# Optimization experiments

Measured on AMD Instinct MI355X. Metric: run time of the kernel, lower is better.

Reference implementation:

```python
import jax, jax.numpy as jnp
import numpy as np

B, H, W, C = 32, 32, 32, 768
E = 4          # num_experts
TOPK = 2
HD = int(C * 0.25)  # 192, expert hidden dim


def setup_inputs() -> dict:
    key = jax.random.key(0)
    ks = jax.random.split(key, 7)
    x = jax.random.normal(ks[0], (B, H, W, C), dtype=jnp.float32)
    # router: nn.Linear(C, E), weight [E, C] init N(0, 0.02), bias zeros
    router_w = jax.random.normal(ks[1], (E, C), dtype=jnp.float32) * 0.02
    router_b = jnp.zeros((E,), dtype=jnp.float32)
    # per-expert MLP: fc1 [E, HD, C], fc2 [E, C, HD] (torch Linear weight layout)
    fc1_w = jax.random.normal(ks[2], (E, HD, C), dtype=jnp.float32) * (1.0 / np.sqrt(C))
    fc1_b = jax.random.normal(ks[3], (E, HD), dtype=jnp.float32) * 0.01
    fc2_w = jax.random.normal(ks[4], (E, C, HD), dtype=jnp.float32) * (1.0 / np.sqrt(HD))
    fc2_b = jax.random.normal(ks[5], (E, C), dtype=jnp.float32) * 0.01
    return {"x": x, "router_w": router_w, "router_b": router_b,
            "fc1_w": fc1_w, "fc1_b": fc1_b, "fc2_w": fc2_w, "fc2_b": fc2_b}


def reference(x, router_w, router_b, fc1_w, fc1_b, fc2_w, fc2_b):
    b, h, w, c = x.shape
    xt = x.reshape(b, h * w, c)                              # [B, S, C]
    # --- router: softmax + top-k + renormalize ---
    logits = jnp.einsum('bsc,ec->bse', xt, router_w) + router_b
    probs = jax.nn.softmax(logits, axis=-1)                  # [B, S, E]
    topk_w, topk_idx = jax.lax.top_k(probs, TOPK)            # [B, S, K]
    topk_w = topk_w / (jnp.sum(topk_w, axis=-1, keepdims=True) + 1e-8)
    # per-expert combine weight: sum over k of weight where idx==e -> [B, S, E]
    combine = jnp.sum(jax.nn.one_hot(topk_idx, E, dtype=xt.dtype)
                      * topk_w[..., None], axis=-2)          # [B, S, E]
    # --- all experts densely (same math as masked gather/scatter) ---
    # fc1 + exact GELU: [B, S, E, HD]
    hmid = jax.nn.gelu(jnp.einsum('bsc,ehc->bseh', xt, fc1_w) + fc1_b,
                       approximate=False)
    # weight tokens before fc2 to avoid [B,S,E,C] intermediate
    hw = hmid * combine[..., None]                           # [B, S, E, HD]
    out = jnp.einsum('bseh,ech->bsc', hw, fc2_w)
    out = out + jnp.einsum('bse,ec->bsc', combine, fc2_b)    # weighted fc2 bias
    return out.reshape(b, h, w, c)
```

## Files before the change

kernel.cpp:

```cpp
#include <hip/hip_runtime.h>
#include <hip/hip_bf16.h>
#include <math.h>

typedef __attribute__((ext_vector_type(8))) __bf16 bf16x8;
typedef __attribute__((ext_vector_type(4))) float f32x4;
typedef __attribute__((ext_vector_type(4))) unsigned short u16x4;

#define TOKENS 32768
#define CDIM   768
#define NKDIM  768

__device__ __forceinline__ void async_copy16(const void* g, void* l) {
    __builtin_amdgcn_global_load_lds(
        (const __attribute__((address_space(1))) void*)g,
        (__attribute__((address_space(3))) void*)l, 16, 0, 0);
}

__device__ __forceinline__ float fast_gelu(float v) {
    float x  = v * 0.70710678118654752f;
    float ax = fabsf(x);
    float t  = __builtin_amdgcn_rcpf(1.0f + 0.3275911f * ax);
    float poly = t * (0.254829592f +
                 t * (-0.284496736f +
                 t * (1.421413741f +
                 t * (-1.453152027f +
                 t * 1.061405429f))));
    float erfv = 1.0f - poly * __expf(-x * x);
    erfv = copysignf(erfv, x);
    return 0.5f * v * (1.0f + erfv);
}

__global__ __launch_bounds__(256) void prep_weights(
    const float* __restrict__ fc1w, const float* __restrict__ fc2w,
    __hip_bfloat16* __restrict__ b1, __hip_bfloat16* __restrict__ b2t)
{
    int idx = blockIdx.x * 256 + threadIdx.x;
    if (idx >= 768 * 768) return;
    b1[idx] = __float2bfloat16(fc1w[idx]);
    int c = idx / 768;
    int r = idx - c * 768;
    int e = r / 192;
    int h = r - e * 192;
    b2t[idx] = __float2bfloat16(fc2w[((size_t)e * 768 + c) * 192 + h]);
}

__global__ __launch_bounds__(256) void router_convert(
    const float* __restrict__ x, const float* __restrict__ rw,
    const float* __restrict__ rb,
    __hip_bfloat16* __restrict__ xb, float* __restrict__ comb)
{
    int wave = threadIdx.x >> 6;
    int lane = threadIdx.x & 63;
    int token = blockIdx.x * 4 + wave;

    const float* xr = x + (size_t)token * CDIM + lane * 12;
    float4 v0 = *(const float4*)(xr);
    float4 v1 = *(const float4*)(xr + 4);
    float4 v2 = *(const float4*)(xr + 8);

    float vals[12];
    *(float4*)(vals) = v0; *(float4*)(vals + 4) = v1; *(float4*)(vals + 8) = v2;
    alignas(16) __hip_bfloat16 hb[12];
#pragma unroll
    for (int j = 0; j < 12; ++j) hb[j] = __float2bfloat16(vals[j]);
    u16x4* dst = (u16x4*)((unsigned short*)xb + (size_t)token * CDIM + lane * 12);
    dst[0] = ((u16x4*)hb)[0];
    dst[1] = ((u16x4*)hb)[1];
    dst[2] = ((u16x4*)hb)[2];

    float s[4];
#pragma unroll
    for (int e = 0; e < 4; ++e) {
        const float* w = rw + e * CDIM + lane * 12;
        float4 w0 = *(const float4*)(w);
        float4 w1 = *(const float4*)(w + 4);
        float4 w2 = *(const float4*)(w + 8);
        s[e] = v0.x * w0.x + v0.y * w0.y + v0.z * w0.z + v0.w * w0.w
             + v1.x * w1.x + v1.y * w1.y + v1.z * w1.z + v1.w * w1.w
             + v2.x * w2.x + v2.y * w2.y + v2.z * w2.z + v2.w * w2.w;
    }
#pragma unroll
    for (int e = 0; e < 4; ++e) {
        float v = s[e];
        v += __shfl_xor(v, 32); v += __shfl_xor(v, 16); v += __shfl_xor(v, 8);
        v += __shfl_xor(v, 4);  v += __shfl_xor(v, 2);  v += __shfl_xor(v, 1);
        s[e] = v;
    }
    float lg[4], p[4];
#pragma unroll
    for (int e = 0; e < 4; ++e) lg[e] = s[e] + rb[e];
    float mx = fmaxf(fmaxf(lg[0], lg[1]), fmaxf(lg[2], lg[3]));
    float ps = 0.f;
#pragma unroll
    for (int e = 0; e < 4; ++e) { p[e] = __expf(lg[e] - mx); ps += p[e]; }
#pragma unroll
    for (int e = 0; e < 4; ++e) p[e] /= ps;
    int a = 0;
#pragma unroll
    for (int e = 1; e < 4; ++e) if (p[e] > p[a]) a = e;
    int b = (a == 0) ? 1 : 0;
#pragma unroll
    for (int e = 0; e < 4; ++e) if (e != a && p[e] > p[b]) b = e;
    float wsum = p[a] + p[b] + 1e-8f;
    float cb[4] = {0.f, 0.f, 0.f, 0.f};
    cb[a] = p[a] / wsum;
    cb[b] = p[b] / wsum;
    if (lane == 0) {
        float4 o; o.x = cb[0]; o.y = cb[1]; o.z = cb[2]; o.w = cb[3];
        *(float4*)(comb + (size_t)token * 4) = o;
    }
}

#define BM 128
#define BN 128
#define BK 64

template <int MODE, int K>
__global__ __launch_bounds__(256) void gemm_bt(
    const __hip_bfloat16* __restrict__ A, const __hip_bfloat16* __restrict__ Bt,
    const float* __restrict__ comb,
    const float* __restrict__ bias1,
    const float* __restrict__ bias2,
    __hip_bfloat16* __restrict__ HW,
    float* __restrict__ OUT)
{
    __shared__ __hip_bfloat16 smem[BM * BK * 4];

    const int tid = threadIdx.x;
    const int wave = tid >> 6, lane = tid & 63;
    const int wm = (wave >> 1) * 64, wn = (wave & 1) * 64;
    const int lrow = lane & 15, quad = lane >> 4;

    const int g = blockIdx.x;
    const int xcd = g & 7;
    const int slot = g >> 3;
    const int byg = slot / 6;
    const int bx = slot - byg * 6;
    const int by = (xcd << 5) + byg;
    const int rowB0 = bx * BN;
    const int rowA0 = by * BM;

    const int srow = lane >> 3;
    const int scol = ((lane & 7) ^ srow) * 8;

    size_t aoff[4];
    __hip_bfloat16* ldsA[4];
#pragma unroll
    for (int p = 0; p < 4; ++p) {
        int c = wave * 4 + p;
        aoff[p] = (size_t)(c * 8 + srow) * K + scol;
        ldsA[p] = smem + c * 8 * BK;
    }
    const __hip_bfloat16* Abase = A + (size_t)rowA0 * K;
    const __hip_bfloat16* Bbase = Bt + (size_t)rowB0 * K;

    auto stage = [&](int buf, int k0) {
        int boff = buf * (2 * BM * BK);
#pragma unroll
        for (int p = 0; p < 4; ++p) {
            async_copy16(Abase + aoff[p] + k0, ldsA[p] + boff);
            async_copy16(Bbase + aoff[p] + k0, ldsA[p] + boff + BM * BK);
        }
    };

    f32x4 acc[4][4] = {};
    constexpr int NIT = K / BK;

    stage(0, 0);
    __syncthreads();
#pragma unroll
    for (int it = 0; it < NIT; ++it) {
        if (it + 1 < NIT) stage((it + 1) & 1, (it + 1) * BK);
        const __hip_bfloat16* As = smem + (it & 1) * (2 * BM * BK);
        const __hip_bfloat16* Bs = As + BM * BK;
#pragma unroll
        for (int kk = 0; kk < BK; kk += 32) {
            bf16x8 af[4], bfr[4];
#pragma unroll
            for (int i = 0; i < 4; ++i) {
                int row = wm + i * 16 + lrow;
                int gp = ((kk >> 3) + quad) ^ (lrow & 7);
                af[i] = *(const bf16x8*)(&As[row * BK + gp * 8]);
            }
#pragma unroll
            for (int j = 0; j < 4; ++j) {
                int row = wn + j * 16 + lrow;
                int gp = ((kk >> 3) + quad) ^ (lrow & 7);
                bfr[j] = *(const bf16x8*)(&Bs[row * BK + gp * 8]);
            }
#pragma unroll
            for (int i = 0; i < 4; ++i)
#pragma unroll
                for (int j = 0; j < 4; ++j)
                    acc[i][j] = __builtin_amdgcn_mfma_f32_16x16x32_bf16(
                        af[i], bfr[j], acc[i][j], 0, 0, 0);
        }
        __syncthreads();
    }

    if (MODE == 0) {
        const int e = (rowB0 + wn) / 192;
        const float* combE = comb + (size_t)rowA0 * 4 + e;
        float b1v[4];
#pragma unroll
        for (int j = 0; j < 4; ++j) b1v[j] = bias1[rowB0 + wn + j * 16 + lrow];
#pragma unroll
        for (int i = 0; i < 4; ++i) {
#pragma unroll
            for (int r = 0; r < 4; ++r) {
                int rowl = wm + i * 16 + quad * 4 + r;
                float c = combE[rowl * 4];
                __hip_bfloat16* srow_p = &smem[rowl * BN + wn + lrow];
#pragma unroll
                for (int j = 0; j < 4; ++j) {
                    float v = fast_gelu(acc[i][j][r] + b1v[j]) * c;
                    srow_p[j * 16] = __float2bfloat16(v);
                }
            }
        }
        __syncthreads();
#pragma unroll
        for (int t = 0; t < 8; ++t) {
            int idx = t * 256 + tid;
            int row = idx >> 4;
            int c16 = (idx & 15) * 8;
            *(uint4*)(HW + (size_t)(rowA0 + row) * NKDIM + rowB0 + c16) =
                *(const uint4*)(&smem[row * BN + c16]);
        }
    } else {
        float4 bbv[4];
#pragma unroll
        for (int j = 0; j < 4; ++j) {
            int col = rowB0 + wn + j * 16 + lrow;
            bbv[j].x = bias2[col];
            bbv[j].y = bias2[768 + col];
            bbv[j].z = bias2[1536 + col];
            bbv[j].w = bias2[2304 + col];
        }
#pragma unroll
        for (int i = 0; i < 4; ++i) {
#pragma unroll
            for (int r = 0; r < 4; ++r) {
                int row = rowA0 + wm + i * 16 + quad * 4 + r;
                float4 cw = *(const float4*)(comb + (size_t)row * 4);
                float* orow = OUT + (size_t)row * CDIM + rowB0 + wn + lrow;
#pragma unroll
                for (int j = 0; j < 4; ++j) {
                    float v = acc[i][j][r]
                            + cw.x * bbv[j].x + cw.y * bbv[j].y
                            + cw.z * bbv[j].z + cw.w * bbv[j].w;
                    orow[j * 16] = v;
                }
            }
        }
    }
}

extern "C" void kernel_launch(void* const* d_in, const int* in_sizes, int n_in,
                              void* d_out, int out_size, void* d_ws, size_t ws_size,
                              hipStream_t stream)
{
    const float* x    = (const float*)d_in[0];
    const float* rw   = (const float*)d_in[1];
    const float* rb   = (const float*)d_in[2];
    const float* fc1w = (const float*)d_in[3];
    const float* fc1b = (const float*)d_in[4];
    const float* fc2w = (const float*)d_in[5];
    const float* fc2b = (const float*)d_in[6];
    float* out = (float*)d_out;

    char* ws = (char*)d_ws;
    __hip_bfloat16* xb  = (__hip_bfloat16*)(ws);
    __hip_bfloat16* hw  = (__hip_bfloat16*)(ws + 50331648);
    __hip_bfloat16* b1  = (__hip_bfloat16*)(ws + 100663296);
    __hip_bfloat16* b2t = (__hip_bfloat16*)(ws + 101842944);
    float*          cmb = (float*)        (ws + 103022592);

    prep_weights<<<2304, 256, 0, stream>>>(fc1w, fc2w, b1, b2t);
    router_convert<<<TOKENS / 4, 256, 0, stream>>>(x, rw, rb, xb, cmb);

    int nblocks = (NKDIM / BN) * (TOKENS / BM);
    gemm_bt<0, CDIM><<<nblocks, 256, 0, stream>>>(xb, b1, cmb, fc1b, nullptr, hw, nullptr);
    gemm_bt<1, NKDIM><<<nblocks, 256, 0, stream>>>(hw, b2t, cmb, nullptr, fc2b, nullptr, out);
}
```

Measured before the change: 287.8 us.

## Group tokens by expert pair and run sparse top-2 GEMMs instead of dense experts

```diff
diff --git a/kernel.cpp b/kernel.cpp
--- a/kernel.cpp
+++ b/kernel.cpp
@@ -8,7 +8,8 @@
 
 #define TOKENS 32768
 #define CDIM   768
-#define NKDIM  768
+#define SLOTCAP 33536
+#define MT_TILES 262
 
 __device__ __forceinline__ void async_copy16(const void* g, void* l) {
     __builtin_amdgcn_global_load_lds(
@@ -30,6 +31,9 @@
     return 0.5f * v * (1.0f + erfv);
 }
 
+__device__ __forceinline__ int pair_lo(int p) { return p < 3 ? 0 : (p < 5 ? 1 : 2); }
+__device__ __forceinline__ int pair_hi(int p) { return p < 3 ? p + 1 : (p < 5 ? p - 1 : 3); }
+
 __global__ __launch_bounds__(256) void prep_weights(
     const float* __restrict__ fc1w, const float* __restrict__ fc2w,
     __hip_bfloat16* __restrict__ b1, __hip_bfloat16* __restrict__ b2t)
@@ -47,8 +51,11 @@
 __global__ __launch_bounds__(256) void router_convert(
     const float* __restrict__ x, const float* __restrict__ rw,
     const float* __restrict__ rb,
-    __hip_bfloat16* __restrict__ xb, float* __restrict__ comb)
-{
+    __hip_bfloat16* __restrict__ xb, float* __restrict__ comb,
+    int* __restrict__ pairid, float2* __restrict__ wpair, int* __restrict__ meta)
+{
+    if (blockIdx.x == 0 && threadIdx.x < 6) meta[threadIdx.x] = 0;
+
     int wave = threadIdx.x >> 6;
     int lane = threadIdx.x & 63;
     int token = blockIdx.x * 4 + wave;
@@ -108,17 +115,70 @@
     if (lane == 0) {
         float4 o; o.x = cb[0]; o.y = cb[1]; o.z = cb[2]; o.w = cb[3];
         *(float4*)(comb + (size_t)token * 4) = o;
-    }
+        int lo = a < b ? a : b;
+        int hi = a < b ? b : a;
+        int pid = (lo == 0) ? hi - 1 : (lo == 1 ? hi + 1 : 5);
+        pairid[token] = pid;
+        wpair[token] = make_float2(cb[lo], cb[hi]);
+    }
+}
+
+__global__ __launch_bounds__(256) void count_prefill(
+    const int* __restrict__ pairid, int* __restrict__ slots,
+    float2* __restrict__ swt, int* __restrict__ meta)
+{
+    __shared__ int sc[6];
+    int tid = threadIdx.x;
+    if (tid < 6) sc[tid] = 0;
+    __syncthreads();
+    int gid = blockIdx.x * 256 + tid;
+    if (gid < SLOTCAP) { slots[gid] = -1; swt[gid] = make_float2(0.f, 0.f); }
+    if (gid < TOKENS) atomicAdd(&sc[pairid[gid]], 1);
+    __syncthreads();
+    if (tid < 6 && sc[tid]) atomicAdd(&meta[tid], sc[tid]);
+}
+
+__global__ void make_offsets(int* __restrict__ meta)
+{
+    if (threadIdx.x == 0) {
+        int run = 0;
+        for (int p = 0; p < 6; ++p) {
+            meta[8 + p]  = run;
+            meta[16 + p] = run;
+            run += ((meta[p] + 127) >> 7) << 7;
+        }
+        meta[14] = run;
+    }
+}
+
+__global__ __launch_bounds__(256) void scatter_tokens(
+    const int* __restrict__ pairid, const float2* __restrict__ wpair,
+    int* __restrict__ slots, float2* __restrict__ swt, int* __restrict__ meta)
+{
+    __shared__ int sc[6], sb[6];
+    int tid = threadIdx.x;
+    if (tid < 6) sc[tid] = 0;
+    __syncthreads();
+    int t = blockIdx.x * 256 + tid;
+    int p = pairid[t];
+    int r = atomicAdd(&sc[p], 1);
+    __syncthreads();
+    if (tid < 6) sb[tid] = sc[tid] ? atomicAdd(&meta[16 + tid], sc[tid]) : 0;
+    __syncthreads();
+    int pos = sb[p] + r;
+    slots[pos] = t;
+    swt[pos] = wpair[t];
 }
 
 #define BM 128
 #define BN 128
 #define BK 64
 
-template <int MODE, int K>
-__global__ __launch_bounds__(256) void gemm_bt(
+template <int MODE, int K, int NT>
+__global__ __launch_bounds__(256) void gemm_moe(
     const __hip_bfloat16* __restrict__ A, const __hip_bfloat16* __restrict__ Bt,
-    const float* __restrict__ comb,
+    const int* __restrict__ slots, const float2* __restrict__ swt,
+    const int* __restrict__ meta, const float* __restrict__ comb,
     const float* __restrict__ bias1,
     const float* __restrict__ bias2,
     __hip_bfloat16* __restrict__ HW,
@@ -131,35 +191,52 @@
     const int wm = (wave >> 1) * 64, wn = (wave & 1) * 64;
     const int lrow = lane & 15, quad = lane >> 4;
 
-    const int g = blockIdx.x;
-    const int xcd = g & 7;
-    const int slot = g >> 3;
-    const int byg = slot / 6;
-    const int bx = slot - byg * 6;
-    const int by = (xcd << 5) + byg;
+    constexpr int nwg = MT_TILES * NT;
+    constexpr int q = nwg >> 3, rr = nwg & 7;
+    const int bid = blockIdx.x;
+    const int xcd = bid & 7, sidx = bid >> 3;
+    const int wg = (xcd < rr ? xcd * (q + 1) : rr * (q + 1) + (xcd - rr) * q) + sidx;
+    const int by = wg / NT;
+    const int bx = wg - by * NT;
     const int rowB0 = bx * BN;
     const int rowA0 = by * BM;
 
+    int pb = 0;
+#pragma unroll
+    for (int i = 1; i < 6; ++i) pb += (rowA0 >= meta[8 + i]) ? 1 : 0;
+    const int lo = pair_lo(pb), hi = pair_hi(pb);
+
     const int srow = lane >> 3;
     const int scol = ((lane & 7) ^ srow) * 8;
 
-    size_t aoff[4];
+    size_t aoff[4], boff[4];
     __hip_bfloat16* ldsA[4];
 #pragma unroll
     for (int p = 0; p < 4; ++p) {
         int c = wave * 4 + p;
-        aoff[p] = (size_t)(c * 8 + srow) * K + scol;
+        int arow = c * 8 + srow;
+        if (MODE == 0) {
+            int tok = slots[rowA0 + arow];
+            tok = tok < 0 ? 0 : tok;
+            aoff[p] = (size_t)tok * K + scol;
+            int grow = rowB0 + arow;
+            int gb = (grow < 192) ? lo * 192 + grow : hi * 192 + (grow - 192);
+            boff[p] = (size_t)gb * K + scol;
+        } else {
+            aoff[p] = (size_t)(rowA0 + arow) * K + scol;
+            boff[p] = (size_t)(rowB0 + arow) * 768 + scol;
+        }
         ldsA[p] = smem + c * 8 * BK;
     }
-    const __hip_bfloat16* Abase = A + (size_t)rowA0 * K;
-    const __hip_bfloat16* Bbase = Bt + (size_t)rowB0 * K;
 
     auto stage = [&](int buf, int k0) {
-        int boff = buf * (2 * BM * BK);
+        int bo = buf * (2 * BM * BK);
+        size_t badd = (MODE == 0) ? (size_t)k0
+                    : (size_t)(k0 < 192 ? lo * 192 : hi * 192 - 192) + k0;
 #pragma unroll
         for (int p = 0; p < 4; ++p) {
-            async_copy16(Abase + aoff[p] + k0, ldsA[p] + boff);
-            async_copy16(Bbase + aoff[p] + k0, ldsA[p] + boff + BM * BK);
+            async_copy16(A + aoff[p] + k0, ldsA[p] + bo);
+            async_copy16(Bt + boff[p] + badd, ldsA[p] + bo + BM * BK);
         }
     };
 
@@ -199,21 +276,25 @@
     }
 
     if (MODE == 0) {
-        const int e = (rowB0 + wn) / 192;
-        const float* combE = comb + (size_t)rowA0 * 4 + e;
+        const bool hf = (rowB0 + wn) >= 192;
         float b1v[4];
 #pragma unroll
-        for (int j = 0; j < 4; ++j) b1v[j] = bias1[rowB0 + wn + j * 16 + lrow];
+        for (int j = 0; j < 4; ++j) {
+            int col = rowB0 + wn + j * 16 + lrow;
+            int ng = (col < 192) ? lo * 192 + col : hi * 192 + (col - 192);
+            b1v[j] = bias1[ng];
+        }
 #pragma unroll
         for (int i = 0; i < 4; ++i) {
 #pragma unroll
             for (int r = 0; r < 4; ++r) {
                 int rowl = wm + i * 16 + quad * 4 + r;
-                float c = combE[rowl * 4];
+                float2 wv = swt[rowA0 + rowl];
+                float cwt = hf ? wv.y : wv.x;
                 __hip_bfloat16* srow_p = &smem[rowl * BN + wn + lrow];
 #pragma unroll
                 for (int j = 0; j < 4; ++j) {
-                    float v = fast_gelu(acc[i][j][r] + b1v[j]) * c;
+                    float v = fast_gelu(acc[i][j][r] + b1v[j]) * cwt;
                     srow_p[j * 16] = __float2bfloat16(v);
                 }
             }
@@ -224,7 +305,7 @@
             int idx = t * 256 + tid;
             int row = idx >> 4;
             int c16 = (idx & 15) * 8;
-            *(uint4*)(HW + (size_t)(rowA0 + row) * NKDIM + rowB0 + c16) =
+            *(uint4*)(HW + (size_t)(rowA0 + row) * 384 + rowB0 + c16) =
                 *(const uint4*)(&smem[row * BN + c16]);
         }
     } else {
@@ -241,9 +322,11 @@
         for (int i = 0; i < 4; ++i) {
 #pragma unroll
             for (int r = 0; r < 4; ++r) {
-                int row = rowA0 + wm + i * 16 + quad * 4 + r;
-                float4 cw = *(const float4*)(comb + (size_t)row * 4);
-                float* orow = OUT + (size_t)row * CDIM + rowB0 + wn + lrow;
+                int slot = rowA0 + wm + i * 16 + quad * 4 + r;
+                int tok = slots[slot];
+                if (tok < 0) continue;
+                float4 cw = *(const float4*)(comb + (size_t)tok * 4);
+                float* orow = OUT + (size_t)tok * CDIM + rowB0 + wn + lrow;
 #pragma unroll
                 for (int j = 0; j < 4; ++j) {
                     float v = acc[i][j][r]
@@ -270,16 +353,25 @@
     float* out = (float*)d_out;
 
     char* ws = (char*)d_ws;
-    __hip_bfloat16* xb  = (__hip_bfloat16*)(ws);
-    __hip_bfloat16* hw  = (__hip_bfloat16*)(ws + 50331648);
-    __hip_bfloat16* b1  = (__hip_bfloat16*)(ws + 100663296);
-    __hip_bfloat16* b2t = (__hip_bfloat16*)(ws + 101842944);
-    float*          cmb = (float*)        (ws + 103022592);
+    __hip_bfloat16* xb   = (__hip_bfloat16*)(ws);
+    __hip_bfloat16* hw   = (__hip_bfloat16*)(ws + 50331648);
+    __hip_bfloat16* b1   = (__hip_bfloat16*)(ws + 76087296);
+    __hip_bfloat16* b2t  = (__hip_bfloat16*)(ws + 77266944);
+    float*          cmb  = (float*)        (ws + 78446592);
+    float2*         wpr  = (float2*)       (ws + 78970880);
+    float2*         swt  = (float2*)       (ws + 79233024);
+    int*            pid  = (int*)          (ws + 79501312);
+    int*            slots= (int*)          (ws + 79632384);
+    int*            meta = (int*)          (ws + 79766528);
 
     prep_weights<<<2304, 256, 0, stream>>>(fc1w, fc2w, b1, b2t);
-    router_convert<<<TOKENS / 4, 256, 0, stream>>>(x, rw, rb, xb, cmb);
-
-    int nblocks = (NKDIM / BN) * (TOKENS / BM);
-    gemm_bt<0, CDIM><<<nblocks, 256, 0, stream>>>(xb, b1, cmb, fc1b, nullptr, hw, nullptr);
-    gemm_bt<1, NKDIM><<<nblocks, 256, 0, stream>>>(hw, b2t, cmb, nullptr, fc2b, nullptr, out);
-}
+    router_convert<<<TOKENS / 4, 256, 0, stream>>>(x, rw, rb, xb, cmb, pid, wpr, meta);
+    count_prefill<<<(SLOTCAP + 255) / 256, 256, 0, stream>>>(pid, slots, swt, meta);
+    make_offsets<<<1, 64, 0, stream>>>(meta);
+    scatter_tokens<<<TOKENS / 256, 256, 0, stream>>>(pid, wpr, slots, swt, meta);
+
+    gemm_moe<0, 768, 3><<<MT_TILES * 3, 256, 0, stream>>>(
+        xb, b1, slots, swt, meta, nullptr, fc1b, nullptr, hw, nullptr);
+    gemm_moe<1, 384, 6><<<MT_TILES * 6, 256, 0, stream>>>(
+        hw, b2t, slots, nullptr, meta, cmb, nullptr, fc2b, nullptr, out);
+}
```

Measured after the change: 289.2 us. Within noise of the previous version (+0.5%).
